# Optimization experiments

Hardware: AMD Instinct MI355X
Metric: run time of the kernel (lower is better)

Reference implementation:

```python
import jax, jax.numpy as jnp
import numpy as np
from jax import lax

B, S, V, E, H = 128, 256, 50000, 300, 512
Hh = H // 2  # per-direction hidden


def _lstm_dir(x, Wih, Whh, bih, bhh):
    # x: [B,S,E] -> hs: [B,S,Hh]; PyTorch gate order i,f,g,o
    b = x.shape[0]
    h0 = jnp.zeros((b, Hh), x.dtype)
    c0 = jnp.zeros((b, Hh), x.dtype)
    bias = bih + bhh

    def step(carry, xt):
        h, c = carry
        g = xt @ Wih.T + h @ Whh.T + bias  # [B,4Hh]
        i, f, gg, o = jnp.split(g, 4, axis=-1)
        c = jax.nn.sigmoid(f) * c + jax.nn.sigmoid(i) * jnp.tanh(gg)
        h = jax.nn.sigmoid(o) * jnp.tanh(c)
        return (h, c), h

    _, hs = lax.scan(step, (h0, c0), jnp.swapaxes(x, 0, 1))
    return jnp.swapaxes(hs, 0, 1)


def _bilstm(x, p):
    fwd = _lstm_dir(x, p['Wih_f'], p['Whh_f'], p['bih_f'], p['bhh_f'])
    bwd = _lstm_dir(jnp.flip(x, 1), p['Wih_b'], p['Whh_b'], p['bih_b'], p['bhh_b'])
    return jnp.concatenate([fwd, jnp.flip(bwd, 1)], axis=-1)  # [B,S,H]


def _masked_mean(h, length_minus1):
    # mean over first (len-1) timesteps, vectorized replacement for per-sample loop
    mask = (jnp.arange(h.shape[1])[None, :] < length_minus1[:, None]).astype(h.dtype)  # [B,S]
    return jnp.einsum('bsh,bs->bh', h, mask) / length_minus1[:, None].astype(h.dtype)


def setup_inputs() -> dict:
    key = jax.random.key(0)
    ks = jax.random.split(key, 20)
    sc = 0.05
    inp = {
        'x1': jax.random.randint(ks[0], (B, S), 0, V, dtype=jnp.int32),
        'x2': jax.random.randint(ks[1], (B, S), 0, V, dtype=jnp.int32),
        'len1': jax.random.randint(ks[2], (B,), 2, S + 1, dtype=jnp.int32),
        'len2': jax.random.randint(ks[3], (B,), 2, S + 1, dtype=jnp.int32),
        'emb': jax.random.normal(ks[4], (V, E), jnp.float32) * sc,
        'Wih_f': jax.random.normal(ks[5], (4 * Hh, E), jnp.float32) * sc,
        'Whh_f': jax.random.normal(ks[6], (4 * Hh, Hh), jnp.float32) * sc,
        'bih_f': jnp.zeros((4 * Hh,), jnp.float32),
        'bhh_f': jnp.zeros((4 * Hh,), jnp.float32),
        'Wih_b': jax.random.normal(ks[7], (4 * Hh, E), jnp.float32) * sc,
        'Whh_b': jax.random.normal(ks[8], (4 * Hh, Hh), jnp.float32) * sc,
        'bih_b': jnp.zeros((4 * Hh,), jnp.float32),
        'bhh_b': jnp.zeros((4 * Hh,), jnp.float32),
        'W1': jax.random.normal(ks[9], (H, H), jnp.float32) * sc,
        'b1': jnp.zeros((H,), jnp.float32),
        'W2': jax.random.normal(ks[10], (H // 2, H), jnp.float32) * sc,
        'b2': jnp.zeros((H // 2,), jnp.float32),
        'Wo': jax.random.normal(ks[11], (1, H // 2), jnp.float32) * sc,
        'bo': jnp.zeros((1,), jnp.float32),
    }
    return inp


def reference(x1, x2, len1, len2, emb, Wih_f, Whh_f, bih_f, bhh_f,
              Wih_b, Whh_b, bih_b, bhh_b, W1, b1, W2, b2, Wo, bo):
    p = dict(Wih_f=Wih_f, Whh_f=Whh_f, bih_f=bih_f, bhh_f=bhh_f,
             Wih_b=Wih_b, Whh_b=Whh_b, bih_b=bih_b, bhh_b=bhh_b)
    e1 = emb[x1]  # [B,S,E]
    e2 = emb[x2]
    h1 = _bilstm(e1, p)  # [B,S,H]
    h2 = _bilstm(e2, p)
    v1 = _masked_mean(h1, len1 - 1)  # [B,H]
    v2 = _masked_mean(h2, len2 - 1)
    vec = jnp.abs(v1 - v2)  # aggr_type == 'sub'
    a1 = jax.nn.relu(vec @ W1.T + b1)
    a2 = jax.nn.relu(a1 @ W2.T + b2)
    logits = (a2 @ Wo.T + bo)[:, 0]  # [B]
    preds = jax.nn.sigmoid(logits)
    return logits, preds
```

## Files before the change

### kernel.cpp

```cpp
#include <hip/hip_runtime.h>
#include <hip/hip_bf16.h>
#include <math.h>

typedef unsigned short u16;
typedef short s16x8 __attribute__((ext_vector_type(8)));
typedef float f32x4v __attribute__((ext_vector_type(4)));
typedef int i32x4 __attribute__((ext_vector_type(4)));
typedef unsigned short u16x4 __attribute__((ext_vector_type(4)));

#define EDIM 300
#define EPAD 320
#define VOCAB 50000

static constexpr size_t SZ_WIH  = (size_t)2 * 1024 * EPAD * 2;
static constexpr size_t SZ_WPK  = (size_t)2 * 1024 * 256;
static constexpr size_t SZ_SW   = (size_t)2 * 1024 * 4;
static constexpr size_t SZ_BIAS = (size_t)2 * 1024 * 4;
static constexpr size_t SZ_HSV  = (size_t)2 * 256 * 256;
static constexpr size_t SZ_CST  = (size_t)2 * 256 * 256 * 4;
static constexpr size_t SZ_VAC  = (size_t)2 * 256 * 256 * 4;
static constexpr size_t SZ_VOUT = (size_t)2 * 128 * 512 * 4;
static constexpr size_t SZ_EMB  = (size_t)VOCAB * EPAD * 2;
static constexpr size_t SZ_PAD  = (size_t)512 * 1024;
static constexpr size_t FIXED_B = SZ_WIH + SZ_WPK + SZ_SW + SZ_BIAS + SZ_HSV + SZ_CST + SZ_VAC + SZ_VOUT + SZ_EMB + SZ_PAD;
static constexpr size_t SZ_STEP = (size_t)2 * 256 * 1024 * 2;


__device__ __forceinline__ float bf2f(u16 u) {
  union { float f; unsigned int i; } v; v.i = ((unsigned int)u) << 16; return v.f;
}
__device__ __forceinline__ u16 f2bf(float f) {
  union { float f; unsigned int i; } v; v.f = f;
  unsigned int r = v.i + 0x7fffu + ((v.i >> 16) & 1u);
  return (u16)(r >> 16);
}
__device__ __forceinline__ void gload_lds16(const void* g, void* l) {
  __builtin_amdgcn_global_load_lds((const __attribute__((address_space(1))) void*)g,
                                   (__attribute__((address_space(3))) void*)l, 16, 0, 0);
}
__device__ __forceinline__ void lds_barrier() {
  asm volatile("s_waitcnt lgkmcnt(0)" ::: "memory");
  __builtin_amdgcn_s_barrier();
}
__device__ __forceinline__ void wave_lds_fence() {
  asm volatile("s_waitcnt lgkmcnt(0)" ::: "memory");
  __builtin_amdgcn_sched_barrier(0);
}
__device__ __forceinline__ void tile_barrier_vm2() {
  asm volatile("s_waitcnt vmcnt(2)" ::: "memory");
  __builtin_amdgcn_s_barrier();
}

__global__ void __launch_bounds__(256)
setup_kernel(const float* __restrict__ emb,
             const float* __restrict__ wih_f, const float* __restrict__ wih_b,
             const float* __restrict__ whh_f, const float* __restrict__ whh_b,
             const float* __restrict__ bih_f, const float* __restrict__ bhh_f,
             const float* __restrict__ bih_b, const float* __restrict__ bhh_b,
             u16* __restrict__ embbf, u16* __restrict__ wih_bf,
             float* __restrict__ bias, char* __restrict__ wpk, float* __restrict__ sw)
{
  const int EMB_BLKS  = (VOCAB * 80 + 255) / 256;
  const int WIH_BLKS  = (2 * 1024 * 80 + 255) / 256;
  const int BIAS_BLKS = 8;
  int b = blockIdx.x;
  int tid = threadIdx.x;

  if (b < EMB_BLKS) {
    int c = b * 256 + tid;
    if (c < VOCAB * 80) {
      int r = c / 80, k4 = (c % 80) * 4;
      u16x4 v = {0, 0, 0, 0};
      if (k4 < EDIM) {
        f32x4v f = *(const f32x4v*)(emb + (size_t)r * EDIM + k4);
        v[0] = f2bf(f[0]); v[1] = f2bf(f[1]); v[2] = f2bf(f[2]); v[3] = f2bf(f[3]);
      }
      *(u16x4*)(embbf + (size_t)r * EPAD + k4) = v;
    }
    return;
  }
  b -= EMB_BLKS;
  if (b < WIH_BLKS) {
    int c = b * 256 + tid;
    if (c < 2 * 1024 * 80) {
      int dp = c / 80, k4 = (c % 80) * 4;
      int d = dp >> 10, p = dp & 1023;
      int w = p >> 7, q = (p >> 4) & 7, ul = p & 15;
      int jlog = (q & 3) * 256 + w * 32 + (q >> 2) * 16 + ul;
      u16x4 v = {0, 0, 0, 0};
      if (k4 < EDIM) {
        f32x4v f = *(const f32x4v*)((d ? wih_b : wih_f) + (size_t)jlog * EDIM + k4);
        v[0] = f2bf(f[0]); v[1] = f2bf(f[1]); v[2] = f2bf(f[2]); v[3] = f2bf(f[3]);
      }
      *(u16x4*)(wih_bf + (size_t)dp * EPAD + k4) = v;
    }
    return;
  }
  b -= WIH_BLKS;
  if (b < BIAS_BLKS) {
    int t2 = b * 256 + tid;
    if (t2 < 2 * 1024) {
      int d = t2 >> 10; int p = t2 & 1023;
      int w = p >> 7, q = (p >> 4) & 7, ul = p & 15;
      int jlog = (q & 3) * 256 + w * 32 + (q >> 2) * 16 + ul;
      bias[t2] = d ? (bih_b[jlog] + bhh_b[jlog]) : (bih_f[jlog] + bhh_f[jlog]);
    }
    return;
  }
  b -= BIAS_BLKS;
  {
    int jp = b * 4 + (tid >> 6);
    if (jp >= 2048) return;
    int t = tid & 63;
    int d = jp >> 10, p = jp & 1023;
    int w = p >> 7, q = (p >> 4) & 7, ul = p & 15;
    int jlog = (q & 3) * 256 + w * 32 + (q >> 2) * 16 + ul;
    const float* src = (d ? whh_b : whh_f) + (size_t)jlog * 256;
    float v[4]; float m = 0.f;
    #pragma unroll
    for (int kk = 0; kk < 4; ++kk) { v[kk] = src[t * 4 + kk]; m = fmaxf(m, fabsf(v[kk])); }
    #pragma unroll
    for (int off = 32; off > 0; off >>= 1) m = fmaxf(m, __shfl_xor(m, off));
    float sunit = m / 127.f;
    if (sunit < 1e-30f) sunit = 1e-30f;
    unsigned int pk = 0;
    #pragma unroll
    for (int kk = 0; kk < 4; ++kk) {
      int qv = (int)rintf(v[kk] / sunit);
      qv = qv > 127 ? 127 : (qv < -127 ? -127 : qv);
      pk |= ((unsigned int)(qv & 255)) << (8 * kk);
    }
    size_t base = ((((size_t)(d * 8 + w) * 8 + q) * 4 + (t >> 4)) * 64
                   + (((t >> 2) & 3) * 16 + ul)) * 16 + (t & 3) * 4;
    *(unsigned int*)&wpk[base] = pk;
    if (t == 0) sw[jp] = sunit / 127.f;
  }
}

__device__ __forceinline__ void gemm_body(
    int bid, const int* __restrict__ x1, const int* __restrict__ x2,
    const u16* __restrict__ embbf, const u16* __restrict__ wih_bf,
    const float* __restrict__ bias, u16* __restrict__ slab,
    int t0, int T, int logT, char* smem)
{
  u16* Bs = (u16*)smem;
  int d  = bid >> (1 + logT);
  int tl = (bid >> 1) & (T - 1);
  int R0 = (bid & 1) * 128;
  int lane = threadIdx.x & 63;
  int w = threadIdx.x >> 6;

  const int* x = (R0 >> 7) ? x2 : x1;
  int t = t0 + tl;
  int tpos = d ? (255 - t) : t;

  int rowR = R0 + w * 16 + (lane & 15);
  int tok = x[(rowR & 127) * 256 + tpos];
  const char* arow = (const char*)embbf + (size_t)tok * 640 + (lane >> 4) * 16;
  s16x8 areg[10];
  #pragma unroll
  for (int kc = 0; kc < 10; ++kc)
    areg[kc] = *(const s16x8*)(arow + kc * 64);

  const char* Bbase = (const char*)(wih_bf + (size_t)d * 1024 * EPAD);
  int ar  = lane >> 3;
  int acb = (lane & 7) * 16;
  int swz = ar << 4;

  #define ISSUE_TILE(nnt, nkt, b3)                                                     \
    { _Pragma("unroll")                                                                \
      for (int i = 0; i < 2; ++i) {                                                    \
        int lrow = (i * 8 + w) * 8 + ar;                                               \
        gload_lds16(Bbase + (size_t)((nnt) * 128 + lrow) * 640 + (nkt) * 128 + (acb ^ swz), \
                    (char*)Bs + (b3) * 16384 + (i * 8 + w) * 1024);                    \
      } }

  ISSUE_TILE(0, 0, 0);
  ISSUE_TILE(0, 1, 1);

  size_t rowbase = (size_t)(d * T + tl) * 256 + R0;
  int ul = lane & 15;

  #pragma unroll
  for (int nt = 0; nt < 8; ++nt) {
    f32x4v acc[8] = {};
    #pragma unroll
    for (int kt = 0; kt < 5; ++kt) {
      const int g = nt * 5 + kt;
      tile_barrier_vm2();
      {
        const int g2 = g + 2;
        if (g2 < 40) ISSUE_TILE(g2 / 5, g2 % 5, g2 % 3);
      }
      const int b3 = g % 3;
      #pragma unroll
      for (int kc2 = 0; kc2 < 2; ++kc2) {
        int cb = kc2 * 64 + (lane >> 4) * 16;
        #pragma unroll
        for (int nf = 0; nf < 8; ++nf) {
          int rr = nf * 16 + (lane & 15);
          s16x8 b = *(const s16x8*)((const char*)Bs + b3 * 16384 + rr * 128 + (cb ^ ((rr & 7) << 4)));
          acc[nf] = __builtin_amdgcn_mfma_f32_16x16x32_bf16(areg[kt * 2 + kc2], b, acc[nf], 0, 0, 0);
        }
      }
    }
    float bv[8];
    #pragma unroll
    for (int nf = 0; nf < 8; ++nf)
      bv[nf] = bias[d * 1024 + nt * 128 + nf * 16 + ul];
    #pragma unroll
    for (int uh = 0; uh < 2; ++uh)
      #pragma unroll
      for (int i = 0; i < 4; ++i) {
        int row = w * 16 + (lane >> 4) * 4 + i;
        u16x4 v;
        #pragma unroll
        for (int g2 = 0; g2 < 4; ++g2)
          v[g2] = f2bf(acc[uh * 4 + g2][i] + bv[uh * 4 + g2]);
        *(u16x4*)(slab + (rowbase + row) * 1024 + nt * 128 + uh * 64 + ul * 4) = v;
      }
  }
  #undef ISSUE_TILE
}

__device__ __forceinline__ void lstm_body(
    int bid, const u16* __restrict__ slab, const i32x4* __restrict__ wpk,
    const float* __restrict__ sw, char* hsave,
    float* cstate, float* vaccst, float* vout,
    const int* __restrict__ len1, const int* __restrict__ len2,
    int t0, int T, char* smem)
{
  char* h = smem;
  int* gst = (int*)(smem + 1152);

  const int d = bid >> 7, bt = bid & 127;
  const int tid = threadIdx.x;
  const int lane = tid & 63, w = tid >> 6;
  const int cl = lane & 15;
  const int cr  = lane >> 5;
  const int cuh = (lane >> 4) & 1;
  const int cu  = w * 32 + cuh * 16 + cl;

  i32x4 bfr[8][4];
  #pragma unroll
  for (int q = 0; q < 8; ++q)
    #pragma unroll
    for (int kc = 0; kc < 4; ++kc)
      bfr[q][kc] = wpk[(((size_t)(d * 8 + w) * 8 + q) * 4 + kc) * 64 + lane];
  float swl4[4];
  #pragma unroll
  for (int g = 0; g < 4; ++g)
    swl4[g] = sw[d * 1024 + w * 128 + (cuh * 4 + g) * 16 + cl];

  const int R0 = bt * 2;
  {
    int r = tid >> 8, u = tid & 255;
    h[r * 288 + u] = (t0 > 0) ? hsave[((size_t)d * 256 + R0 + r) * 256 + u] : (char)0;
  }

  const int RR = R0 + cr;
  const int lm = ((RR >> 7) ? len2 : len1)[RR & 127] - 1;
  const size_t sidx = ((size_t)d * 256 + RR) * 256 + cu;
  float c = 0.f, va = 0.f;
  if (t0 > 0) { c = cstate[sidx]; va = vaccst[sidx]; }

  const size_t GSTEP = (size_t)256 * 1024;
  const u16* gcell = slab + ((size_t)d * T * 256 + RR) * 1024 + w * 128 + cuh * 64 + cl * 4;
  u16x4 gv = *(const u16x4*)gcell;
  __syncthreads();

  const bool final_chunk = (t0 + T == 256);
  int par = 0;

  for (int tl = 0; tl < T; ++tl) {
    u16x4 gvn = *(const u16x4*)(gcell + GSTEP * (size_t)(tl + 1));

    i32x4 a[4] = {{0,0,0,0},{0,0,0,0},{0,0,0,0},{0,0,0,0}};
    if (cl < 2) {
      #pragma unroll
      for (int kc = 0; kc < 4; ++kc)
        a[kc] = *(const i32x4*)&h[(par * 2 + cl) * 288 + kc * 64 + (lane >> 4) * 16];
    }
    i32x4 acc[8];
    #pragma unroll
    for (int q = 0; q < 8; ++q) {
      i32x4 z = {0, 0, 0, 0};
      #pragma unroll
      for (int kc = 0; kc < 4; ++kc)
        z = __builtin_amdgcn_mfma_i32_16x16x64_i8(a[kc], bfr[q][kc], z, 0, 0, 0);
      acc[q] = z;
    }

    if (lane < 16) {
      #pragma unroll
      for (int r2 = 0; r2 < 2; ++r2)
        #pragma unroll
        for (int uh2 = 0; uh2 < 2; ++uh2) {
          i32x4 v = { acc[uh2 * 4 + 0][r2], acc[uh2 * 4 + 1][r2],
                      acc[uh2 * 4 + 2][r2], acc[uh2 * 4 + 3][r2] };
          *(i32x4*)&gst[(w * 64 + r2 * 32 + uh2 * 16 + lane) * 4] = v;
        }
    }
    wave_lds_fence();
    i32x4 g4 = *(const i32x4*)&gst[(w * 64 + lane) * 4];

    {
      float s0 = (float)g4[0] * swl4[0] + bf2f(gv[0]);
      float s1 = (float)g4[1] * swl4[1] + bf2f(gv[1]);
      float s2 = (float)g4[2] * swl4[2] + bf2f(gv[2]);
      float s3 = (float)g4[3] * swl4[3] + bf2f(gv[3]);
      float I = __builtin_amdgcn_rcpf(1.f + __expf(-s0));
      float F = __builtin_amdgcn_rcpf(1.f + __expf(-s1));
      float G = 1.f - 2.f * __builtin_amdgcn_rcpf(__expf(2.f * s2) + 1.f);
      float O = __builtin_amdgcn_rcpf(1.f + __expf(-s3));
      float cn = F * c + I * G;
      c = cn;
      float hn = O * (1.f - 2.f * __builtin_amdgcn_rcpf(__expf(2.f * cn) + 1.f));
      int tmap = d ? (255 - (t0 + tl)) : (t0 + tl);
      if (tmap < lm) va += hn;
      h[((par ^ 1) * 2 + cr) * 288 + cu] = (char)(int)rintf(hn * 127.f);
    }
    lds_barrier();
    gv = gvn;
    par ^= 1;
  }

  cstate[sidx] = c;
  vaccst[sidx] = va;
  if (final_chunk) {
    vout[((size_t)(RR >> 7) * 128 + (RR & 127)) * 512 + d * 256 + cu] = va / (float)lm;
  } else {
    int r = tid >> 8, u = tid & 255;
    hsave[((size_t)d * 256 + R0 + r) * 256 + u] = h[(par * 2 + r) * 288 + u];
  }
}

__global__ void __launch_bounds__(512, 2)
fused_kernel(const int* x1, const int* x2, const u16* embbf, const u16* wih_bf,
             const float* bias, const i32x4* wpk, const float* sw,
             char* hsave, float* cstate, float* vaccst, float* vout,
             const int* len1, const int* len2,
             const u16* lstm_slab, u16* gemm_slab,
             int lstm_t0, int gemm_t0, int nL, int T, int logT)
{
  __shared__ __align__(16) char smem[49152];
  if ((int)blockIdx.x < nL) {
    lstm_body(blockIdx.x, lstm_slab, wpk, sw, hsave, cstate, vaccst, vout,
              len1, len2, lstm_t0, T, smem);
  } else if (gemm_t0 >= 0) {
    gemm_body(blockIdx.x - nL, x1, x2, embbf, wih_bf, bias, gemm_slab,
              gemm_t0, T, logT, smem);
  }
}

__global__ void mlp_kernel(const float* v, const float* W1, const float* b1,
                           const float* W2, const float* b2, const float* Wo, const float* bo,
                           float* out)
{
  __shared__ float vec[512];
  __shared__ float a1[512];
  __shared__ float red[4];
  int b = blockIdx.x;
  int tid = threadIdx.x;
  for (int i = tid; i < 512; i += 256)
    vec[i] = fabsf(v[(size_t)b * 512 + i] - v[(size_t)(128 + b) * 512 + i]);
  __syncthreads();
  for (int j = tid; j < 512; j += 256) {
    float s = b1[j];
    const float* wr = W1 + (size_t)j * 512;
    for (int k = 0; k < 512; ++k) s += vec[k] * wr[k];
    a1[j] = fmaxf(s, 0.f);
  }
  __syncthreads();
  float s = b2[tid];
  {
    const float* wr = W2 + (size_t)tid * 512;
    for (int k = 0; k < 512; ++k) s += a1[k] * wr[k];
  }
  float p = fmaxf(s, 0.f) * Wo[tid];
  for (int off = 32; off > 0; off >>= 1) p += __shfl_down(p, off);
  if ((tid & 63) == 0) red[tid >> 6] = p;
  __syncthreads();
  if (tid == 0) {
    float logit = red[0] + red[1] + red[2] + red[3] + bo[0];
    out[b] = logit;
    out[128 + b] = 1.f / (1.f + __expf(-logit));
  }
}

extern "C" void kernel_launch(void* const* d_in, const int* in_sizes, int n_in,
                              void* d_out, int out_size, void* d_ws, size_t ws_size,
                              hipStream_t stream)
{
  const int*   x1    = (const int*)d_in[0];
  const int*   x2    = (const int*)d_in[1];
  const int*   len1  = (const int*)d_in[2];
  const int*   len2  = (const int*)d_in[3];
  const float* emb   = (const float*)d_in[4];
  const float* wih_f = (const float*)d_in[5];
  const float* whh_f = (const float*)d_in[6];
  const float* bih_f = (const float*)d_in[7];
  const float* bhh_f = (const float*)d_in[8];
  const float* wih_b = (const float*)d_in[9];
  const float* whh_b = (const float*)d_in[10];
  const float* bih_b = (const float*)d_in[11];
  const float* bhh_b = (const float*)d_in[12];
  const float* W1    = (const float*)d_in[13];
  const float* b1    = (const float*)d_in[14];
  const float* W2    = (const float*)d_in[15];
  const float* b2    = (const float*)d_in[16];
  const float* Wo    = (const float*)d_in[17];
  const float* bo    = (const float*)d_in[18];

  char* p = (char*)d_ws;
  u16*   wih_bf = (u16*)p;          p += SZ_WIH;
  char*  wpk    = (char*)p;         p += SZ_WPK;
  float* swp    = (float*)p;        p += SZ_SW;
  float* bias   = (float*)p;        p += SZ_BIAS;
  char*  hsave  = (char*)p;         p += SZ_HSV;
  float* cst    = (float*)p;        p += SZ_CST;
  float* vac    = (float*)p;        p += SZ_VAC;
  float* vout   = (float*)p;        p += SZ_VOUT;
  u16*   embbf  = (u16*)p;          p += SZ_EMB;

  int T = 128;
  while (T > 1 && FIXED_B + (size_t)2 * T * SZ_STEP > ws_size) T >>= 1;
  int logT = __builtin_ctz((unsigned)T);
  u16* slab0 = (u16*)p;             p += (size_t)T * SZ_STEP;
  u16* slab1 = (u16*)p;
  u16* slabs[2] = { slab0, slab1 };

  {
    const int EMB_BLKS  = (VOCAB * 80 + 255) / 256;
    const int WIH_BLKS  = (2 * 1024 * 80 + 255) / 256;
    const int BIAS_BLKS = 8;
    const int WHH_BLKS  = 512;
    int total_blocks = EMB_BLKS + WIH_BLKS + BIAS_BLKS + WHH_BLKS;
    setup_kernel<<<total_blocks, 256, 0, stream>>>(
        emb, wih_f, wih_b, whh_f, whh_b, bih_f, bhh_f, bih_b, bhh_b,
        embbf, wih_bf, bias, wpk, swp);
  }

  int NCH = 256 / T;
  fused_kernel<<<4 * T, 512, 0, stream>>>(x1, x2, embbf, wih_bf, bias,
                                          (const i32x4*)wpk, swp, hsave, cst, vac, vout,
                                          len1, len2, slabs[0], slabs[0],
                                          -1, 0, 0, T, logT);
  for (int ch = 1; ch < NCH; ++ch) {
    fused_kernel<<<256 + 4 * T, 512, 0, stream>>>(x1, x2, embbf, wih_bf, bias,
                                                  (const i32x4*)wpk, swp, hsave, cst, vac, vout,
                                                  len1, len2, slabs[(ch - 1) & 1], slabs[ch & 1],
                                                  (ch - 1) * T, ch * T, 256, T, logT);
  }
  fused_kernel<<<256, 512, 0, stream>>>(x1, x2, embbf, wih_bf, bias,
                                        (const i32x4*)wpk, swp, hsave, cst, vac, vout,
                                        len1, len2, slabs[(NCH - 1) & 1], slabs[0],
                                        (NCH - 1) * T, -1, 256, T, logT);

  mlp_kernel<<<128, 256, 0, stream>>>(vout, W1, b1, W2, b2, Wo, bo, (float*)d_out);
}
```

Before: 423.5 us.

## Fuse embedding bf16 conversion into the input GEMM gather and deepen tile pipeline

Drops the setup pass that converts the whole 50000x300 embedding table to padded bf16. The GEMM now gathers fp32 rows straight from the original table and converts only the tokens it uses into registers. The B-tile LDS ring grows from 3 to 4 buffers, with three tiles in flight and a vmcnt(4) wait. This saves a large read/write pass over the vocabulary, at the cost of more shared memory per block (64KB), which may lower occupancy, and some unaligned scalar loads for the tail of each embedding row.

```diff
diff --git a/kernel.cpp b/kernel.cpp
--- a/kernel.cpp
+++ b/kernel.cpp
@@ -20,9 +20,8 @@
 static constexpr size_t SZ_CST  = (size_t)2 * 256 * 256 * 4;
 static constexpr size_t SZ_VAC  = (size_t)2 * 256 * 256 * 4;
 static constexpr size_t SZ_VOUT = (size_t)2 * 128 * 512 * 4;
-static constexpr size_t SZ_EMB  = (size_t)VOCAB * EPAD * 2;
 static constexpr size_t SZ_PAD  = (size_t)512 * 1024;
-static constexpr size_t FIXED_B = SZ_WIH + SZ_WPK + SZ_SW + SZ_BIAS + SZ_HSV + SZ_CST + SZ_VAC + SZ_VOUT + SZ_EMB + SZ_PAD;
+static constexpr size_t FIXED_B = SZ_WIH + SZ_WPK + SZ_SW + SZ_BIAS + SZ_HSV + SZ_CST + SZ_VAC + SZ_VOUT + SZ_PAD;
 static constexpr size_t SZ_STEP = (size_t)2 * 256 * 1024 * 2;
 
 
@@ -46,40 +45,24 @@
   asm volatile("s_waitcnt lgkmcnt(0)" ::: "memory");
   __builtin_amdgcn_sched_barrier(0);
 }
-__device__ __forceinline__ void tile_barrier_vm2() {
-  asm volatile("s_waitcnt vmcnt(2)" ::: "memory");
+__device__ __forceinline__ void tile_barrier_vm4() {
+  asm volatile("s_waitcnt vmcnt(4)" ::: "memory");
   __builtin_amdgcn_s_barrier();
 }
 
 __global__ void __launch_bounds__(256)
-setup_kernel(const float* __restrict__ emb,
-             const float* __restrict__ wih_f, const float* __restrict__ wih_b,
+setup_kernel(const float* __restrict__ wih_f, const float* __restrict__ wih_b,
              const float* __restrict__ whh_f, const float* __restrict__ whh_b,
              const float* __restrict__ bih_f, const float* __restrict__ bhh_f,
              const float* __restrict__ bih_b, const float* __restrict__ bhh_b,
-             u16* __restrict__ embbf, u16* __restrict__ wih_bf,
-             float* __restrict__ bias, char* __restrict__ wpk, float* __restrict__ sw)
-{
-  const int EMB_BLKS  = (VOCAB * 80 + 255) / 256;
+             u16* __restrict__ wih_bf, float* __restrict__ bias,
+             char* __restrict__ wpk, float* __restrict__ sw)
+{
   const int WIH_BLKS  = (2 * 1024 * 80 + 255) / 256;
   const int BIAS_BLKS = 8;
   int b = blockIdx.x;
   int tid = threadIdx.x;
 
-  if (b < EMB_BLKS) {
-    int c = b * 256 + tid;
-    if (c < VOCAB * 80) {
-      int r = c / 80, k4 = (c % 80) * 4;
-      u16x4 v = {0, 0, 0, 0};
-      if (k4 < EDIM) {
-        f32x4v f = *(const f32x4v*)(emb + (size_t)r * EDIM + k4);
-        v[0] = f2bf(f[0]); v[1] = f2bf(f[1]); v[2] = f2bf(f[2]); v[3] = f2bf(f[3]);
-      }
-      *(u16x4*)(embbf + (size_t)r * EPAD + k4) = v;
-    }
-    return;
-  }
-  b -= EMB_BLKS;
   if (b < WIH_BLKS) {
     int c = b * 256 + tid;
     if (c < 2 * 1024 * 80) {
@@ -139,7 +122,7 @@
 
 __device__ __forceinline__ void gemm_body(
     int bid, const int* __restrict__ x1, const int* __restrict__ x2,
-    const u16* __restrict__ embbf, const u16* __restrict__ wih_bf,
+    const float* __restrict__ emb, const u16* __restrict__ wih_bf,
     const float* __restrict__ bias, u16* __restrict__ slab,
     int t0, int T, int logT, char* smem)
 {
@@ -154,29 +137,46 @@
   int t = t0 + tl;
   int tpos = d ? (255 - t) : t;
 
-  int rowR = R0 + w * 16 + (lane & 15);
-  int tok = x[(rowR & 127) * 256 + tpos];
-  const char* arow = (const char*)embbf + (size_t)tok * 640 + (lane >> 4) * 16;
-  s16x8 areg[10];
-  #pragma unroll
-  for (int kc = 0; kc < 10; ++kc)
-    areg[kc] = *(const s16x8*)(arow + kc * 64);
-
   const char* Bbase = (const char*)(wih_bf + (size_t)d * 1024 * EPAD);
   int ar  = lane >> 3;
   int acb = (lane & 7) * 16;
   int swz = ar << 4;
 
-  #define ISSUE_TILE(nnt, nkt, b3)                                                     \
+  #define ISSUE_TILE(nnt, nkt, b4)                                                     \
     { _Pragma("unroll")                                                                \
       for (int i = 0; i < 2; ++i) {                                                    \
         int lrow = (i * 8 + w) * 8 + ar;                                               \
         gload_lds16(Bbase + (size_t)((nnt) * 128 + lrow) * 640 + (nkt) * 128 + (acb ^ swz), \
-                    (char*)Bs + (b3) * 16384 + (i * 8 + w) * 1024);                    \
+                    (char*)Bs + (b4) * 16384 + (i * 8 + w) * 1024);                    \
       } }
 
   ISSUE_TILE(0, 0, 0);
   ISSUE_TILE(0, 1, 1);
+  ISSUE_TILE(0, 2, 2);
+
+  int rowR = R0 + w * 16 + (lane & 15);
+  int tok = x[(rowR & 127) * 256 + tpos];
+  const float* arowf = emb + (size_t)tok * EDIM + (lane >> 4) * 8;
+  s16x8 areg[10];
+  #pragma unroll
+  for (int kc = 0; kc < 9; ++kc) {
+    f32x4v f0 = *(const f32x4v*)(arowf + kc * 32);
+    f32x4v f1 = *(const f32x4v*)(arowf + kc * 32 + 4);
+    s16x8 v;
+    v[0] = (short)f2bf(f0[0]); v[1] = (short)f2bf(f0[1]);
+    v[2] = (short)f2bf(f0[2]); v[3] = (short)f2bf(f0[3]);
+    v[4] = (short)f2bf(f1[0]); v[5] = (short)f2bf(f1[1]);
+    v[6] = (short)f2bf(f1[2]); v[7] = (short)f2bf(f1[3]);
+    areg[kc] = v;
+  }
+  {
+    int k0 = 288 + (lane >> 4) * 8;
+    s16x8 v;
+    #pragma unroll
+    for (int j = 0; j < 8; ++j)
+      v[j] = (k0 + j < EDIM) ? (short)f2bf(emb[(size_t)tok * EDIM + k0 + j]) : (short)0;
+    areg[9] = v;
+  }
 
   size_t rowbase = (size_t)(d * T + tl) * 256 + R0;
   int ul = lane & 15;
@@ -187,19 +187,19 @@
     #pragma unroll
     for (int kt = 0; kt < 5; ++kt) {
       const int g = nt * 5 + kt;
-      tile_barrier_vm2();
+      tile_barrier_vm4();
       {
-        const int g2 = g + 2;
-        if (g2 < 40) ISSUE_TILE(g2 / 5, g2 % 5, g2 % 3);
+        const int g3 = g + 3;
+        if (g3 < 40) ISSUE_TILE(g3 / 5, g3 % 5, g3 % 4);
       }
-      const int b3 = g % 3;
+      const int b4 = g % 4;
       #pragma unroll
       for (int kc2 = 0; kc2 < 2; ++kc2) {
         int cb = kc2 * 64 + (lane >> 4) * 16;
         #pragma unroll
         for (int nf = 0; nf < 8; ++nf) {
           int rr = nf * 16 + (lane & 15);
-          s16x8 b = *(const s16x8*)((const char*)Bs + b3 * 16384 + rr * 128 + (cb ^ ((rr & 7) << 4)));
+          s16x8 b = *(const s16x8*)((const char*)Bs + b4 * 16384 + rr * 128 + (cb ^ ((rr & 7) << 4)));
           acc[nf] = __builtin_amdgcn_mfma_f32_16x16x32_bf16(areg[kt * 2 + kc2], b, acc[nf], 0, 0, 0);
         }
       }
@@ -336,19 +336,19 @@
 }
 
 __global__ void __launch_bounds__(512, 2)
-fused_kernel(const int* x1, const int* x2, const u16* embbf, const u16* wih_bf,
+fused_kernel(const int* x1, const int* x2, const float* emb, const u16* wih_bf,
              const float* bias, const i32x4* wpk, const float* sw,
              char* hsave, float* cstate, float* vaccst, float* vout,
              const int* len1, const int* len2,
              const u16* lstm_slab, u16* gemm_slab,
              int lstm_t0, int gemm_t0, int nL, int T, int logT)
 {
-  __shared__ __align__(16) char smem[49152];
+  __shared__ __align__(16) char smem[65536];
   if ((int)blockIdx.x < nL) {
     lstm_body(blockIdx.x, lstm_slab, wpk, sw, hsave, cstate, vaccst, vout,
               len1, len2, lstm_t0, T, smem);
   } else if (gemm_t0 >= 0) {
-    gemm_body(blockIdx.x - nL, x1, x2, embbf, wih_bf, bias, gemm_slab,
+    gemm_body(blockIdx.x - nL, x1, x2, emb, wih_bf, bias, gemm_slab,
               gemm_t0, T, logT, smem);
   }
 }
@@ -421,7 +421,6 @@
   float* cst    = (float*)p;        p += SZ_CST;
   float* vac    = (float*)p;        p += SZ_VAC;
   float* vout   = (float*)p;        p += SZ_VOUT;
-  u16*   embbf  = (u16*)p;          p += SZ_EMB;
 
   int T = 128;
   while (T > 1 && FIXED_B + (size_t)2 * T * SZ_STEP > ws_size) T >>= 1;
@@ -431,28 +430,26 @@
   u16* slabs[2] = { slab0, slab1 };
 
   {
-    const int EMB_BLKS  = (VOCAB * 80 + 255) / 256;
     const int WIH_BLKS  = (2 * 1024 * 80 + 255) / 256;
     const int BIAS_BLKS = 8;
     const int WHH_BLKS  = 512;
-    int total_blocks = EMB_BLKS + WIH_BLKS + BIAS_BLKS + WHH_BLKS;
-    setup_kernel<<<total_blocks, 256, 0, stream>>>(
-        emb, wih_f, wih_b, whh_f, whh_b, bih_f, bhh_f, bih_b, bhh_b,
-        embbf, wih_bf, bias, wpk, swp);
+    setup_kernel<<<WIH_BLKS + BIAS_BLKS + WHH_BLKS, 256, 0, stream>>>(
+        wih_f, wih_b, whh_f, whh_b, bih_f, bhh_f, bih_b, bhh_b,
+        wih_bf, bias, wpk, swp);
   }
 
   int NCH = 256 / T;
-  fused_kernel<<<4 * T, 512, 0, stream>>>(x1, x2, embbf, wih_bf, bias,
+  fused_kernel<<<4 * T, 512, 0, stream>>>(x1, x2, emb, wih_bf, bias,
                                           (const i32x4*)wpk, swp, hsave, cst, vac, vout,
                                           len1, len2, slabs[0], slabs[0],
                                           -1, 0, 0, T, logT);
   for (int ch = 1; ch < NCH; ++ch) {
-    fused_kernel<<<256 + 4 * T, 512, 0, stream>>>(x1, x2, embbf, wih_bf, bias,
+    fused_kernel<<<256 + 4 * T, 512, 0, stream>>>(x1, x2, emb, wih_bf, bias,
                                                   (const i32x4*)wpk, swp, hsave, cst, vac, vout,
                                                   len1, len2, slabs[(ch - 1) & 1], slabs[ch & 1],
                                                   (ch - 1) * T, ch * T, 256, T, logT);
   }
-  fused_kernel<<<256, 512, 0, stream>>>(x1, x2, embbf, wih_bf, bias,
+  fused_kernel<<<256, 512, 0, stream>>>(x1, x2, emb, wih_bf, bias,
                                         (const i32x4*)wpk, swp, hsave, cst, vac, vout,
                                         len1, len2, slabs[(NCH - 1) & 1], slabs[0],
                                         (NCH - 1) * T, -1, 256, T, logT);
```

New measurement: 425.2 us (median of 2 runs). Within noise of the previous version (+0.4%).
